# Performance work log

Hardware: AMD Instinct MI355X
Metric: run time of the kernel (lower is better)

Reference implementation:

```python
import jax, jax.numpy as jnp
import numpy as np

DIM = 512
HID = 4 * DIM
EPS = 1e-5


def _layernorm(x, g, b):
    mu = jnp.mean(x, axis=-1, keepdims=True)
    var = jnp.mean(jnp.square(x - mu), axis=-1, keepdims=True)
    return (x - mu) * jax.lax.rsqrt(var + EPS) * g + b


def setup_inputs() -> dict:
    key = jax.random.key(0)
    ks = jax.random.split(key, 16)
    s = 1.0 / np.sqrt(DIM)
    sh = 1.0 / np.sqrt(HID)
    inp = {
        "x": jax.random.normal(ks[0], (4, 4096, DIM), dtype=jnp.float32),
        "ln1_g": jnp.ones((DIM,), jnp.float32),
        "ln1_b": jnp.zeros((DIM,), jnp.float32),
        "Wq": jax.random.normal(ks[1], (DIM, DIM), jnp.float32) * s,
        "bq": jnp.zeros((DIM,), jnp.float32),
        "Wk": jax.random.normal(ks[2], (DIM, DIM), jnp.float32) * s,
        "bk": jnp.zeros((DIM,), jnp.float32),
        "Wv": jax.random.normal(ks[3], (DIM, DIM), jnp.float32) * s,
        "bv": jnp.zeros((DIM,), jnp.float32),
        "Wo": jax.random.normal(ks[4], (DIM, DIM), jnp.float32) * s,
        "bo": jnp.zeros((DIM,), jnp.float32),
        "ln2_g": jnp.ones((DIM,), jnp.float32),
        "ln2_b": jnp.zeros((DIM,), jnp.float32),
        "W1": jax.random.normal(ks[5], (DIM, HID), jnp.float32) * s,
        "b1": jnp.zeros((HID,), jnp.float32),
        "W2": jax.random.normal(ks[6], (HID, DIM), jnp.float32) * sh,
        "b2": jnp.zeros((DIM,), jnp.float32),
    }
    return inp


def reference(x, ln1_g, ln1_b, Wq, bq, Wk, bk, Wv, bv, Wo, bo, ln2_g, ln2_b, W1, b1, W2, b2):
    # Pre-norm self attention (single head, naive softmax(QK^T)V)
    h = _layernorm(x, ln1_g, ln1_b)
    q = h @ Wq + bq  # [B,S,D]
    k = h @ Wk + bk
    v = h @ Wv + bv
    scale = q.shape[-1] ** (-0.5)
    scores = jnp.einsum("bsd,btd->bst", q, k) * scale  # [B,S,S]
    attn = jax.nn.softmax(scores, axis=-1)
    o = jnp.einsum("bst,btd->bsd", attn, v) @ Wo + bo
    x = x + o
    # Pre-norm GELU MLP (exact erf gelu, matching torch F.gelu default)
    h2 = _layernorm(x, ln2_g, ln2_b)
    m = jax.nn.gelu(h2 @ W1 + b1, approximate=False) @ W2 + b2
    return x + m
```

## Files before the change

### kernel.cpp

```cpp
#include <hip/hip_runtime.h>

typedef unsigned short u16;
typedef float f32x4 __attribute__((ext_vector_type(4)));
typedef __bf16 bf16x8 __attribute__((ext_vector_type(8)));

__device__ __forceinline__ u16 f2bf(float f) {
  unsigned u = __float_as_uint(f);
  u += 0x7fffu + ((u >> 16) & 1u);
  return (u16)(u >> 16);
}

__device__ __forceinline__ f32x4 mfma16(bf16x8 a, bf16x8 b, f32x4 c) {
  return __builtin_amdgcn_mfma_f32_16x16x32_bf16(a, b, c, 0, 0, 0);
}

#define GLDS16(gp, lp)                                                            \
  __builtin_amdgcn_global_load_lds((const __attribute__((address_space(1))) void*)(gp), \
                                   (__attribute__((address_space(3))) void*)(lp), 16, 0, 0)

__global__ void pack_bias_k(const float* __restrict__ bq, const float* __restrict__ bk,
                            const float* __restrict__ bv, float* __restrict__ bqkv) {
  int i = blockIdx.x * 256 + threadIdx.x;
  if (i < 512) bqkv[i] = bq[i];
  else if (i < 1024) bqkv[i] = bk[i - 512];
  else if (i < 1536) bqkv[i] = bv[i - 1024];
}

__global__ void tconv_w(const float* __restrict__ in, u16* __restrict__ out, int R, int C) {
  __shared__ float t[32][33];
  int c0 = blockIdx.x * 32, r0 = blockIdx.y * 32;
  int tx = threadIdx.x, ty = threadIdx.y;
#pragma unroll
  for (int j = 0; j < 4; ++j)
    t[ty * 4 + j][tx] = in[(size_t)(r0 + ty * 4 + j) * C + c0 + tx];
  __syncthreads();
#pragma unroll
  for (int j = 0; j < 4; ++j)
    out[(size_t)(c0 + ty * 4 + j) * R + r0 + tx] = f2bf(t[tx][ty * 4 + j]);
}

__global__ void tpose_v(const u16* __restrict__ qkv, u16* __restrict__ Vt) {
  __shared__ u16 t[32][41];
  int b = blockIdx.z;
  int c0 = blockIdx.x * 32, r0 = blockIdx.y * 32;
  int tx = threadIdx.x, ty = threadIdx.y;
  const u16* in = qkv + (size_t)b * 4096 * 1536 + 1024;
  u16* outp = Vt + (size_t)b * 512 * 4096;
#pragma unroll
  for (int j = 0; j < 4; ++j)
    t[ty * 4 + j][tx] = in[(size_t)(r0 + ty * 4 + j) * 1536 + c0 + tx];
  __syncthreads();
#pragma unroll
  for (int j = 0; j < 4; ++j)
    outp[(size_t)(c0 + ty * 4 + j) * 4096 + r0 + tx] = t[tx][ty * 4 + j];
}

__global__ __launch_bounds__(256) void ln_fwd(const float* __restrict__ x,
                                              const float* __restrict__ gw,
                                              const float* __restrict__ bw,
                                              u16* __restrict__ out) {
  int row = blockIdx.x * 4 + (threadIdx.x >> 6);
  int lane = threadIdx.x & 63;
  const float* xr = x + (size_t)row * 512;
  float xv[8], gv[8], bv[8];
  *(float4*)&xv[0] = *(const float4*)(xr + lane * 8);
  *(float4*)&xv[4] = *(const float4*)(xr + lane * 8 + 4);
  *(float4*)&gv[0] = *(const float4*)(gw + lane * 8);
  *(float4*)&gv[4] = *(const float4*)(gw + lane * 8 + 4);
  *(float4*)&bv[0] = *(const float4*)(bw + lane * 8);
  *(float4*)&bv[4] = *(const float4*)(bw + lane * 8 + 4);
  float sum = 0.f, sq = 0.f;
#pragma unroll
  for (int j = 0; j < 8; ++j) { sum += xv[j]; sq += xv[j] * xv[j]; }
#pragma unroll
  for (int d = 1; d < 64; d <<= 1) {
    sum += __shfl_xor(sum, d);
    sq += __shfl_xor(sq, d);
  }
  float mean = sum * (1.f / 512.f);
  float var = sq * (1.f / 512.f) - mean * mean;
  float rstd = rsqrtf(var + 1e-5f);
  union { uint4 u; u16 h[8]; } ob;
#pragma unroll
  for (int j = 0; j < 8; ++j)
    ob.h[j] = f2bf((xv[j] - mean) * rstd * gv[j] + bv[j]);
  *(uint4*)(out + (size_t)row * 512 + lane * 8) = ob.u;
}

template <int EPI>
__global__ __launch_bounds__(256, 2) void gemm_bt(const u16* __restrict__ A, int lda, size_t sA,
                                                  const u16* __restrict__ Bt, int ldb, size_t sB,
                                                  const float* __restrict__ bias,
                                                  const float* __restrict__ res,
                                                  void* __restrict__ out, int ldc, size_t sC,
                                                  int M, int N, int K) {
  __shared__ u16 As[128 * 64];
  __shared__ u16 Bs[128 * 64];
  const int tid = threadIdx.x;
  const int lane = tid & 63, w = tid >> 6;
  const int wr = w >> 1, wc = w & 1;
  const int m0 = blockIdx.x * 128, n0 = blockIdx.y * 128;
  const int lh = lane >> 4, ll = lane & 15;
  A += (size_t)blockIdx.z * sA;
  Bt += (size_t)blockIdx.z * sB;

  const int srow = lane >> 2;
  const int scol = (lane & 3) * 8;
  const u16* ga = A + (size_t)(m0 + srow) * lda + scol;
  const u16* gb = Bt + (size_t)(n0 + srow) * ldb + scol;

  bf16x8 ones;
#pragma unroll
  for (int j = 0; j < 8; ++j) ones[j] = (__bf16)1.0f;

  f32x4 acc[4][4] = {};
  f32x4 accs[4] = {};
  const int nk = K >> 6;
  for (int kt = 0; kt < nk; ++kt) {
    const int k0 = kt << 6;
#pragma unroll
    for (int j = 0; j < 4; ++j) {
      const int t = w * 4 + j;
      const int radd = (t & 7) * 16;
      const int kadd = (t >> 3) * 32;
      GLDS16(ga + (size_t)radd * lda + k0 + kadd, &As[t * 512]);
      GLDS16(gb + (size_t)radd * ldb + k0 + kadd, &Bs[t * 512]);
    }
    __syncthreads();
#pragma unroll
    for (int ks = 0; ks < 2; ++ks) {
      bf16x8 a[4], b[4];
#pragma unroll
      for (int m = 0; m < 4; ++m)
        a[m] = *(const bf16x8*)&As[ks * 4096 + (wr * 64 + m * 16 + ll) * 32 + lh * 8];
#pragma unroll
      for (int n = 0; n < 4; ++n)
        b[n] = *(const bf16x8*)&Bs[ks * 4096 + (wc * 64 + n * 16 + ll) * 32 + lh * 8];
#pragma unroll
      for (int m = 0; m < 4; ++m)
#pragma unroll
        for (int n = 0; n < 4; ++n)
          acc[m][n] = mfma16(a[m], b[n], acc[m][n]);
      if (EPI == 4) {
#pragma unroll
        for (int m = 0; m < 4; ++m) accs[m] = mfma16(a[m], ones, accs[m]);
      }
    }
    __syncthreads();
  }

  u16* outh = (u16*)out + (size_t)blockIdx.z * sC;
  float* outf = (float*)out + (size_t)blockIdx.z * sC;
#pragma unroll
  for (int m = 0; m < 4; ++m) {
    int row = m0 + wr * 64 + m * 16 + lh * 4;
#pragma unroll
    for (int n = 0; n < 4; ++n) {
      int col = n0 + wc * 64 + n * 16 + ll;
      float bv = (EPI == 1 || EPI == 2 || EPI == 3) ? bias[col] : 0.f;
#pragma unroll
      for (int i = 0; i < 4; ++i) {
        float v = acc[m][n][i] + bv;
        size_t idx = (size_t)(row + i) * ldc + col;
        if (EPI == 2) {
          float y = 0.7978845608028654f * (v + 0.044715f * v * v * v);
          v = v / (1.f + __expf(-2.f * y));
        }
        if (EPI == 4) v = v * (1.f / accs[m][i]);
        if (EPI == 5) v = __expf(v * 0.044194173824159216f);
        if (EPI == 3)
          outf[idx] = v + res[(size_t)blockIdx.z * sC + idx];
        else
          outh[idx] = f2bf(v);
      }
    }
  }
}

extern "C" void kernel_launch(void* const* d_in, const int* in_sizes, int n_in,
                              void* d_out, int out_size, void* d_ws, size_t ws_size,
                              hipStream_t stream) {
  const float* x     = (const float*)d_in[0];
  const float* ln1g  = (const float*)d_in[1];
  const float* ln1b  = (const float*)d_in[2];
  const float* Wq    = (const float*)d_in[3];
  const float* bq    = (const float*)d_in[4];
  const float* Wk    = (const float*)d_in[5];
  const float* bk    = (const float*)d_in[6];
  const float* Wv    = (const float*)d_in[7];
  const float* bv    = (const float*)d_in[8];
  const float* Wo    = (const float*)d_in[9];
  const float* bo    = (const float*)d_in[10];
  const float* ln2g  = (const float*)d_in[11];
  const float* ln2b  = (const float*)d_in[12];
  const float* W1    = (const float*)d_in[13];
  const float* b1    = (const float*)d_in[14];
  const float* W2    = (const float*)d_in[15];
  const float* b2    = (const float*)d_in[16];

  char* base = (char*)d_ws;
  u16* Wqkvt = (u16*)base;
  u16* Wot   = Wqkvt + 786432;
  u16* W1t   = Wot + 262144;
  u16* W2t   = W1t + 1048576;
  float* bqkv = (float*)(W2t + 1048576);
  u16* qkvb = (u16*)(base + (8ull << 20));
  u16* Vt   = qkvb + (size_t)16384 * 1536;
  u16* m1   = qkvb;
  u16* hb   = (u16*)(base + (72ull << 20));
  const size_t sco_off = 88ull << 20;
  u16* scores = (u16*)(base + sco_off);
  float* x1 = (float*)scores;

  const size_t S = 4096;
  const size_t per_b = S * S * 2;
  int nb = 1;
  if (ws_size >= sco_off + 4 * per_b) nb = 4;
  else if (ws_size >= sco_off + 2 * per_b) nb = 2;

  dim3 tb(32, 8);
  pack_bias_k<<<6, 256, 0, stream>>>(bq, bk, bv, bqkv);
  tconv_w<<<dim3(16, 16), tb, 0, stream>>>(Wq, Wqkvt, 512, 512);
  tconv_w<<<dim3(16, 16), tb, 0, stream>>>(Wk, Wqkvt + 262144, 512, 512);
  tconv_w<<<dim3(16, 16), tb, 0, stream>>>(Wv, Wqkvt + 524288, 512, 512);
  tconv_w<<<dim3(16, 16), tb, 0, stream>>>(Wo, Wot, 512, 512);
  tconv_w<<<dim3(64, 16), tb, 0, stream>>>(W1, W1t, 512, 2048);
  tconv_w<<<dim3(16, 64), tb, 0, stream>>>(W2, W2t, 2048, 512);

  ln_fwd<<<4096, 256, 0, stream>>>(x, ln1g, ln1b, hb);
  gemm_bt<1><<<dim3(128, 12, 1), 256, 0, stream>>>(hb, 512, 0, Wqkvt, 512, 0, bqkv, nullptr,
                                                   qkvb, 1536, 0, 16384, 1536, 512);
  tpose_v<<<dim3(16, 128, 4), tb, 0, stream>>>(qkvb, Vt);

  for (int b0 = 0; b0 < 4; b0 += nb) {
    int nz = (4 - b0) < nb ? (4 - b0) : nb;
    const u16* qk = qkvb + (size_t)b0 * S * 1536;
    gemm_bt<5><<<dim3(32, 32, nz), 256, 0, stream>>>(qk, 1536, S * 1536, qk + 512, 1536, S * 1536,
                                                     nullptr, nullptr, scores, 4096, S * S,
                                                     4096, 4096, 512);
    gemm_bt<4><<<dim3(32, 4, nz), 256, 0, stream>>>(scores, 4096, S * S,
                                                    Vt + (size_t)b0 * 512 * S, 4096, 512 * S,
                                                    nullptr, nullptr,
                                                    hb + (size_t)b0 * S * 512, 512, S * 512,
                                                    4096, 512, 4096);
  }

  gemm_bt<3><<<dim3(128, 4, 1), 256, 0, stream>>>(hb, 512, 0, Wot, 512, 0, bo, x,
                                                  x1, 512, 0, 16384, 512, 512);
  ln_fwd<<<4096, 256, 0, stream>>>(x1, ln2g, ln2b, hb);
  gemm_bt<2><<<dim3(128, 16, 1), 256, 0, stream>>>(hb, 512, 0, W1t, 512, 0, b1, nullptr,
                                                   m1, 2048, 0, 16384, 2048, 512);
  gemm_bt<3><<<dim3(128, 4, 1), 256, 0, stream>>>(m1, 2048, 0, W2t, 2048, 0, b2, x1,
                                                  (float*)d_out, 512, 0, 16384, 512, 2048);
}
```

Before: 375.4 us.

## Fuse V transpose into QKV GEMM epilogue and merge weight prep kernels

The QKV projection epilogue now writes the V columns directly in transposed layout into Vt and selects the q/k/v bias per column. This removes the separate V transpose kernel and the bias-packing kernel. The six weight transpose/convert launches are merged into one block-indexed kernel to cut launch overhead. The transposed V stores are strided 8-byte writes, which may coalesce poorly.

```diff
diff --git a/kernel.cpp b/kernel.cpp
--- a/kernel.cpp
+++ b/kernel.cpp
@@ -18,18 +18,34 @@
   __builtin_amdgcn_global_load_lds((const __attribute__((address_space(1))) void*)(gp), \
                                    (__attribute__((address_space(3))) void*)(lp), 16, 0, 0)
 
-__global__ void pack_bias_k(const float* __restrict__ bq, const float* __restrict__ bk,
-                            const float* __restrict__ bv, float* __restrict__ bqkv) {
-  int i = blockIdx.x * 256 + threadIdx.x;
-  if (i < 512) bqkv[i] = bq[i];
-  else if (i < 1024) bqkv[i] = bk[i - 512];
-  else if (i < 1536) bqkv[i] = bv[i - 1024];
-}
-
-__global__ void tconv_w(const float* __restrict__ in, u16* __restrict__ out, int R, int C) {
+__global__ __launch_bounds__(256) void prep_all(const float* __restrict__ Wq,
+                                                const float* __restrict__ Wk,
+                                                const float* __restrict__ Wv,
+                                                const float* __restrict__ Wo,
+                                                const float* __restrict__ W1,
+                                                const float* __restrict__ W2,
+                                                u16* __restrict__ Wqkvt, u16* __restrict__ Wot,
+                                                u16* __restrict__ W1t, u16* __restrict__ W2t) {
   __shared__ float t[32][33];
-  int c0 = blockIdx.x * 32, r0 = blockIdx.y * 32;
-  int tx = threadIdx.x, ty = threadIdx.y;
+  const int bid = blockIdx.x;
+  const float* in;
+  u16* out;
+  int R, C, bx, by;
+  if (bid < 256) {
+    in = Wq; out = Wqkvt; R = 512; C = 512; bx = bid & 15; by = bid >> 4;
+  } else if (bid < 512) {
+    in = Wk; out = Wqkvt + 262144; R = 512; C = 512; bx = (bid - 256) & 15; by = (bid - 256) >> 4;
+  } else if (bid < 768) {
+    in = Wv; out = Wqkvt + 524288; R = 512; C = 512; bx = (bid - 512) & 15; by = (bid - 512) >> 4;
+  } else if (bid < 1024) {
+    in = Wo; out = Wot; R = 512; C = 512; bx = (bid - 768) & 15; by = (bid - 768) >> 4;
+  } else if (bid < 2048) {
+    in = W1; out = W1t; R = 512; C = 2048; bx = (bid - 1024) & 63; by = (bid - 1024) >> 6;
+  } else {
+    in = W2; out = W2t; R = 2048; C = 512; bx = (bid - 2048) & 15; by = (bid - 2048) >> 4;
+  }
+  const int c0 = bx * 32, r0 = by * 32;
+  const int tx = threadIdx.x & 31, ty = threadIdx.x >> 5;
 #pragma unroll
   for (int j = 0; j < 4; ++j)
     t[ty * 4 + j][tx] = in[(size_t)(r0 + ty * 4 + j) * C + c0 + tx];
@@ -37,22 +53,6 @@
 #pragma unroll
   for (int j = 0; j < 4; ++j)
     out[(size_t)(c0 + ty * 4 + j) * R + r0 + tx] = f2bf(t[tx][ty * 4 + j]);
-}
-
-__global__ void tpose_v(const u16* __restrict__ qkv, u16* __restrict__ Vt) {
-  __shared__ u16 t[32][41];
-  int b = blockIdx.z;
-  int c0 = blockIdx.x * 32, r0 = blockIdx.y * 32;
-  int tx = threadIdx.x, ty = threadIdx.y;
-  const u16* in = qkv + (size_t)b * 4096 * 1536 + 1024;
-  u16* outp = Vt + (size_t)b * 512 * 4096;
-#pragma unroll
-  for (int j = 0; j < 4; ++j)
-    t[ty * 4 + j][tx] = in[(size_t)(r0 + ty * 4 + j) * 1536 + c0 + tx];
-  __syncthreads();
-#pragma unroll
-  for (int j = 0; j < 4; ++j)
-    outp[(size_t)(c0 + ty * 4 + j) * 4096 + r0 + tx] = t[tx][ty * 4 + j];
 }
 
 __global__ __launch_bounds__(256) void ln_fwd(const float* __restrict__ x,
@@ -91,7 +91,10 @@
 __global__ __launch_bounds__(256, 2) void gemm_bt(const u16* __restrict__ A, int lda, size_t sA,
                                                   const u16* __restrict__ Bt, int ldb, size_t sB,
                                                   const float* __restrict__ bias,
+                                                  const float* __restrict__ bias1,
+                                                  const float* __restrict__ bias2,
                                                   const float* __restrict__ res,
+                                                  u16* __restrict__ vtg,
                                                   void* __restrict__ out, int ldc, size_t sC,
                                                   int M, int N, int K) {
   __shared__ u16 As[128 * 64];
@@ -157,21 +160,35 @@
 #pragma unroll
     for (int n = 0; n < 4; ++n) {
       int col = n0 + wc * 64 + n * 16 + ll;
-      float bv = (EPI == 1 || EPI == 2 || EPI == 3) ? bias[col] : 0.f;
-#pragma unroll
-      for (int i = 0; i < 4; ++i) {
-        float v = acc[m][n][i] + bv;
-        size_t idx = (size_t)(row + i) * ldc + col;
-        if (EPI == 2) {
-          float y = 0.7978845608028654f * (v + 0.044715f * v * v * v);
-          v = v / (1.f + __expf(-2.f * y));
+      float bv = 0.f;
+      if (EPI == 1) {
+        const float* bp = (col < 512) ? bias : (col < 1024 ? bias1 : bias2);
+        bv = bp[col & 511];
+      } else if (EPI == 2 || EPI == 3) {
+        bv = bias[col];
+      }
+      if (EPI == 1 && col >= 1024) {
+        union { uint2 u; u16 h[4]; } pk;
+#pragma unroll
+        for (int i = 0; i < 4; ++i) pk.h[i] = f2bf(acc[m][n][i] + bv);
+        const int b = row >> 12, brow = row & 4095;
+        *(uint2*)&vtg[((size_t)(b * 512 + (col - 1024))) * 4096 + brow] = pk.u;
+      } else {
+#pragma unroll
+        for (int i = 0; i < 4; ++i) {
+          float v = acc[m][n][i] + bv;
+          size_t idx = (size_t)(row + i) * ldc + col;
+          if (EPI == 2) {
+            float y = 0.7978845608028654f * (v + 0.044715f * v * v * v);
+            v = v / (1.f + __expf(-2.f * y));
+          }
+          if (EPI == 4) v = v * (1.f / accs[m][i]);
+          if (EPI == 5) v = __expf(v * 0.044194173824159216f);
+          if (EPI == 3)
+            outf[idx] = v + res[(size_t)blockIdx.z * sC + idx];
+          else
+            outh[idx] = f2bf(v);
         }
-        if (EPI == 4) v = v * (1.f / accs[m][i]);
-        if (EPI == 5) v = __expf(v * 0.044194173824159216f);
-        if (EPI == 3)
-          outf[idx] = v + res[(size_t)blockIdx.z * sC + idx];
-        else
-          outh[idx] = f2bf(v);
       }
     }
   }
@@ -188,7 +205,7 @@
   const float* Wk    = (const float*)d_in[5];
   const float* bk    = (const float*)d_in[6];
   const float* Wv    = (const float*)d_in[7];
-  const float* bv    = (const float*)d_in[8];
+  const float* bVv   = (const float*)d_in[8];
   const float* Wo    = (const float*)d_in[9];
   const float* bo    = (const float*)d_in[10];
   const float* ln2g  = (const float*)d_in[11];
@@ -203,7 +220,6 @@
   u16* Wot   = Wqkvt + 786432;
   u16* W1t   = Wot + 262144;
   u16* W2t   = W1t + 1048576;
-  float* bqkv = (float*)(W2t + 1048576);
   u16* qkvb = (u16*)(base + (8ull << 20));
   u16* Vt   = qkvb + (size_t)16384 * 1536;
   u16* m1   = qkvb;
@@ -218,38 +234,34 @@
   if (ws_size >= sco_off + 4 * per_b) nb = 4;
   else if (ws_size >= sco_off + 2 * per_b) nb = 2;
 
-  dim3 tb(32, 8);
-  pack_bias_k<<<6, 256, 0, stream>>>(bq, bk, bv, bqkv);
-  tconv_w<<<dim3(16, 16), tb, 0, stream>>>(Wq, Wqkvt, 512, 512);
-  tconv_w<<<dim3(16, 16), tb, 0, stream>>>(Wk, Wqkvt + 262144, 512, 512);
-  tconv_w<<<dim3(16, 16), tb, 0, stream>>>(Wv, Wqkvt + 524288, 512, 512);
-  tconv_w<<<dim3(16, 16), tb, 0, stream>>>(Wo, Wot, 512, 512);
-  tconv_w<<<dim3(64, 16), tb, 0, stream>>>(W1, W1t, 512, 2048);
-  tconv_w<<<dim3(16, 64), tb, 0, stream>>>(W2, W2t, 2048, 512);
+  prep_all<<<3072, 256, 0, stream>>>(Wq, Wk, Wv, Wo, W1, W2, Wqkvt, Wot, W1t, W2t);
 
   ln_fwd<<<4096, 256, 0, stream>>>(x, ln1g, ln1b, hb);
-  gemm_bt<1><<<dim3(128, 12, 1), 256, 0, stream>>>(hb, 512, 0, Wqkvt, 512, 0, bqkv, nullptr,
+  gemm_bt<1><<<dim3(128, 12, 1), 256, 0, stream>>>(hb, 512, 0, Wqkvt, 512, 0,
+                                                   bq, bk, bVv, nullptr, Vt,
                                                    qkvb, 1536, 0, 16384, 1536, 512);
-  tpose_v<<<dim3(16, 128, 4), tb, 0, stream>>>(qkvb, Vt);
 
   for (int b0 = 0; b0 < 4; b0 += nb) {
     int nz = (4 - b0) < nb ? (4 - b0) : nb;
     const u16* qk = qkvb + (size_t)b0 * S * 1536;
     gemm_bt<5><<<dim3(32, 32, nz), 256, 0, stream>>>(qk, 1536, S * 1536, qk + 512, 1536, S * 1536,
-                                                     nullptr, nullptr, scores, 4096, S * S,
-                                                     4096, 4096, 512);
+                                                     nullptr, nullptr, nullptr, nullptr, nullptr,
+                                                     scores, 4096, S * S, 4096, 4096, 512);
     gemm_bt<4><<<dim3(32, 4, nz), 256, 0, stream>>>(scores, 4096, S * S,
                                                     Vt + (size_t)b0 * 512 * S, 4096, 512 * S,
-                                                    nullptr, nullptr,
+                                                    nullptr, nullptr, nullptr, nullptr, nullptr,
                                                     hb + (size_t)b0 * S * 512, 512, S * 512,
                                                     4096, 512, 4096);
   }
 
-  gemm_bt<3><<<dim3(128, 4, 1), 256, 0, stream>>>(hb, 512, 0, Wot, 512, 0, bo, x,
+  gemm_bt<3><<<dim3(128, 4, 1), 256, 0, stream>>>(hb, 512, 0, Wot, 512, 0,
+                                                  bo, nullptr, nullptr, x, nullptr,
                                                   x1, 512, 0, 16384, 512, 512);
   ln_fwd<<<4096, 256, 0, stream>>>(x1, ln2g, ln2b, hb);
-  gemm_bt<2><<<dim3(128, 16, 1), 256, 0, stream>>>(hb, 512, 0, W1t, 512, 0, b1, nullptr,
+  gemm_bt<2><<<dim3(128, 16, 1), 256, 0, stream>>>(hb, 512, 0, W1t, 512, 0,
+                                                   b1, nullptr, nullptr, nullptr, nullptr,
                                                    m1, 2048, 0, 16384, 2048, 512);
-  gemm_bt<3><<<dim3(128, 4, 1), 256, 0, stream>>>(m1, 2048, 0, W2t, 2048, 0, b2, x1,
+  gemm_bt<3><<<dim3(128, 4, 1), 256, 0, stream>>>(m1, 2048, 0, W2t, 2048, 0,
+                                                  b2, nullptr, nullptr, x1, nullptr,
                                                   (float*)d_out, 512, 0, 16384, 512, 2048);
 }
```

Measured after the change: 352.9 us. -6.0%, faster.
